# Kernel optimization log

Hardware: AMD Instinct MI355X
Metric: run time of the kernel (lower is better)

The kernel has to match this reference:

```python
import jax, jax.numpy as jnp
import numpy as np

EMBED_DIM = 1024
NUM_HEADS = 16
HEAD_DIM = EMBED_DIM // NUM_HEADS
B, T = 4, 1024
NEG = -1.0e9
LN_EPS = 1e-5


def setup_inputs() -> dict:
    key = jax.random.key(0)
    ks = jax.random.split(key, 13)
    s = 1.0 / np.sqrt(EMBED_DIM)
    return {
        "query": jax.random.normal(ks[0], (B, T, EMBED_DIM), jnp.float32),
        "key": jax.random.normal(ks[1], (B, T, EMBED_DIM), jnp.float32),
        "value": jax.random.normal(ks[2], (B, T, EMBED_DIM), jnp.float32),
        "mask": jax.random.randint(ks[3], (B, 1, T, T), 0, 2, jnp.int32),
        "Wq": jax.random.normal(ks[4], (EMBED_DIM, EMBED_DIM), jnp.float32) * s,
        "bq": jnp.zeros((EMBED_DIM,), jnp.float32),
        "Wk": jax.random.normal(ks[5], (EMBED_DIM, EMBED_DIM), jnp.float32) * s,
        "bk": jnp.zeros((EMBED_DIM,), jnp.float32),
        "Wv": jax.random.normal(ks[6], (EMBED_DIM, EMBED_DIM), jnp.float32) * s,
        "bv": jnp.zeros((EMBED_DIM,), jnp.float32),
        "Wo": jax.random.normal(ks[7], (EMBED_DIM, EMBED_DIM), jnp.float32) * s,
        "bo": jnp.zeros((EMBED_DIM,), jnp.float32),
        "gamma": jnp.ones((EMBED_DIM,), jnp.float32),
        "beta": jnp.zeros((EMBED_DIM,), jnp.float32),
    }


def _split_heads(x):
    # (B, T, E) -> (B, H, T, D)
    b, t, _ = x.shape
    return x.reshape(b, t, NUM_HEADS, HEAD_DIM).transpose(0, 2, 1, 3)


def _mha(query, key, value, mask, Wq, bq, Wk, bk, Wv, bv, Wo, bo, gamma, beta,
         temperature=1.0):
    q = _split_heads(query @ Wq.T + bq)
    k = _split_heads(key @ Wk.T + bk)
    v = _split_heads(value @ Wv.T + bv)
    # scores: (B, H, T, T)
    scale = jnp.sqrt(jnp.float32(HEAD_DIM)) * temperature
    scores = jnp.einsum("bhqd,bhkd->bhqk", q, k) / scale
    scores = jnp.where(mask == 0, NEG, scores)
    scores = scores - jnp.max(scores, axis=-1, keepdims=True)
    # temperature >= 0.01 in this config, so the low-temperature hard-cutoff
    # branch is skipped (matches torch's Python-level `if temperature < 0.01`).
    scores = jnp.nan_to_num(scores, nan=0.0, posinf=1.0e9, neginf=-1.0e9)
    attn = jax.nn.softmax(scores, axis=-1)
    # eval mode: dropout is identity (self.training is False)
    out = jnp.einsum("bhqk,bhkd->bhqd", attn, v)  # (B, H, T, D)
    out = out.transpose(0, 2, 1, 3).reshape(query.shape[0], query.shape[1], EMBED_DIM)
    out = out @ Wo.T + bo
    # layer norm over embed_dim
    mu = jnp.mean(out, axis=-1, keepdims=True)
    var = jnp.mean(jnp.square(out - mu), axis=-1, keepdims=True)
    out = (out - mu) * jax.lax.rsqrt(var + LN_EPS) * gamma + beta
    return out


def reference(query, key, value, mask, Wq, bq, Wk, bk, Wv, bv, Wo, bo, gamma, beta):
    return _mha(query, key, value, mask, Wq, bq, Wk, bk, Wv, bv, Wo, bo, gamma, beta)
```

## Files before the change

### kernel.cpp

```cpp
#include <hip/hip_runtime.h>
#include <cmath>

#define T_SEQ 1024
#define EMB   1024
#define NH    16
#define HD    64
#define NB    4
#define BQ    64
#define BK    64

#define QSCALE 0.18033688011112042f
#define BIAS2  -1.44269504e9f

using frag8   = __attribute__((ext_vector_type(8))) short;
using f32x4   = __attribute__((ext_vector_type(4))) float;
using short4v = __attribute__((ext_vector_type(4))) short;
using short8v = __attribute__((ext_vector_type(8))) short;

__device__ inline short f2bf(float f) {
    union { float f; unsigned u; } x; x.f = f;
    unsigned r = (x.u + 0x7FFFu + ((x.u >> 16) & 1u)) >> 16;
    return (short)r;
}
__device__ inline short f2bf_rhu(float f) {
    union { float f; unsigned u; } x; x.f = f;
    return (short)((x.u + 0x8000u) >> 16);
}
__device__ inline float bf2f(unsigned short u) {
    union { unsigned u; float f; } x; x.u = ((unsigned)u) << 16;
    return x.f;
}

__device__ inline void glds16(const short* g, short* l) {
    __builtin_amdgcn_global_load_lds(
        (const __attribute__((address_space(1))) void*)g,
        (__attribute__((address_space(3))) void*)l, 16, 0, 0);
}

struct ConvArgs { const float* src[7]; short* dst[7]; int n8[7]; };

__global__ __launch_bounds__(256) void convert_bf16(ConvArgs a) {
    const int y = blockIdx.y;
    const int t = blockIdx.x * 256 + threadIdx.x;
    if (t >= a.n8[y]) return;
    const float4* s = (const float4*)a.src[y];
    const float4 v0 = s[t * 2], v1 = s[t * 2 + 1];
    short8v o;
    o[0] = f2bf(v0.x); o[1] = f2bf(v0.y); o[2] = f2bf(v0.z); o[3] = f2bf(v0.w);
    o[4] = f2bf(v1.x); o[5] = f2bf(v1.y); o[6] = f2bf(v1.z); o[7] = f2bf(v1.w);
    *(short8v*)&a.dst[y][t * 8] = o;
}

__global__ __launch_bounds__(256) void convert_mask(
    const int* __restrict__ mask, short* __restrict__ dst)
{
    const int wave = threadIdx.x >> 6, lane = threadIdx.x & 63;
    const int tile = blockIdx.x * 4 + wave;
    const int bb   = tile >> 12;
    const int q16  = (tile >> 6) & 63;
    const int k16  = tile & 63;
    const int qrow = lane >> 2;
    const int col4 = (lane & 3) * 4;
    const int4 mv = *(const int4*)&mask[((size_t)bb * T_SEQ + q16 * 16 + qrow) * T_SEQ
                                        + k16 * 16 + col4];
    const short BB = f2bf(BIAS2);
    short4v o;
    o[0] = mv.x ? (short)0 : BB;
    o[1] = mv.y ? (short)0 : BB;
    o[2] = mv.z ? (short)0 : BB;
    o[3] = mv.w ? (short)0 : BB;
    *(short4v*)&dst[(size_t)tile * 256 + qrow * 16 + col4] = o;
}

struct GemmB { const short* A; const short* W; const float* bias; short* out; float scale; };
struct QkvArgs { GemmB g[3]; };

template <int MODE>
__device__ inline void gemm_core(const short* __restrict__ A,
                                 const short* __restrict__ W,
                                 const float* __restrict__ bias,
                                 float scale,
                                 short* __restrict__ outS,
                                 float* __restrict__ outF,
                                 int m0, int n0)
{
    __shared__ short As[2][128 * 32];
    __shared__ short Bs[2][128 * 32];

    const int tid  = threadIdx.x;
    const int wave = tid >> 6;
    const int lane = tid & 63;
    const int quad = lane >> 4;
    const int lm   = lane & 15;
    const int wr   = wave >> 1;
    const int wc   = wave & 1;
    const int K    = EMB;

    const int G0 = wave * 64 + lane, G1 = G0 + 256;
    const short* aSrc0 = A + (size_t)(m0 + (G0 >> 2)) * K + (G0 & 3) * 8;
    const short* aSrc1 = A + (size_t)(m0 + (G1 >> 2)) * K + (G1 & 3) * 8;
    const short* bSrc0 = W + (size_t)(n0 + (G0 >> 2)) * K + (G0 & 3) * 8;
    const short* bSrc1 = W + (size_t)(n0 + (G1 >> 2)) * K + (G1 & 3) * 8;
    short* aDst0 = &As[0][wave * 512];
    short* aDst1 = &As[0][2048 + wave * 512];
    short* bDst0 = &Bs[0][wave * 512];
    short* bDst1 = &Bs[0][2048 + wave * 512];

    f32x4 acc[4][4];
#pragma unroll
    for (int i = 0; i < 4; ++i)
#pragma unroll
        for (int j = 0; j < 4; ++j) acc[i][j] = (f32x4){0.f, 0.f, 0.f, 0.f};

    for (int kk = 0; kk < K; kk += 64) {
        __syncthreads();
        glds16(aSrc0 + kk,      aDst0);
        glds16(aSrc1 + kk,      aDst1);
        glds16(bSrc0 + kk,      bDst0);
        glds16(bSrc1 + kk,      bDst1);
        glds16(aSrc0 + kk + 32, aDst0 + 4096);
        glds16(aSrc1 + kk + 32, aDst1 + 4096);
        glds16(bSrc0 + kk + 32, bDst0 + 4096);
        glds16(bSrc1 + kk + 32, bDst1 + 4096);
        __syncthreads();

#pragma unroll
        for (int p = 0; p < 2; ++p) {
            frag8 aF[4], bF[4];
#pragma unroll
            for (int i = 0; i < 4; ++i)
                aF[i] = *(const frag8*)&As[p][(wr * 64 + i * 16 + lm) * 32 + quad * 8];
#pragma unroll
            for (int j = 0; j < 4; ++j)
                bF[j] = *(const frag8*)&Bs[p][(wc * 64 + j * 16 + lm) * 32 + quad * 8];
#pragma unroll
            for (int i = 0; i < 4; ++i)
#pragma unroll
                for (int j = 0; j < 4; ++j)
                    acc[i][j] = __builtin_amdgcn_mfma_f32_16x16x32_bf16(
                        aF[i], bF[j], acc[i][j], 0, 0, 0);
        }
    }

#pragma unroll
    for (int i = 0; i < 4; ++i)
#pragma unroll
        for (int j = 0; j < 4; ++j) {
            const int n = n0 + wc * 64 + j * 16 + lm;
            const float bv = bias[n];
#pragma unroll
            for (int rr = 0; rr < 4; ++rr) {
                const int m = m0 + wr * 64 + i * 16 + quad * 4 + rr;
                const float val = (acc[i][j][rr] + bv) * scale;
                if (MODE == 0) {
                    outF[((size_t)(m >> 4) * 64 + (n >> 4)) * 256 +
                         rr * 64 + quad * 16 + lm] = val;
                } else {
                    const int bb = m >> 10, tt = m & 1023;
                    const int h = n >> 6,  d  = n & 63;
                    const size_t bh = (size_t)bb * NH + h;
                    if (MODE == 1) {
                        outS[((bh * 64 + (tt >> 4)) * 8 + (d >> 3)) * 128 +
                             (tt & 15) * 8 + (d & 7)] = f2bf(val);
                    } else {
                        outS[((((bh * 16 + (tt >> 6)) * 2 + ((tt >> 5) & 1)) * 4 +
                              (d >> 4)) * 4 + ((tt >> 3) & 3)) * 128 +
                             (d & 15) * 8 + (tt & 7)] = f2bf(val);
                    }
                }
            }
        }
}

__global__ __launch_bounds__(256, 3) void gemm_qkv(QkvArgs args) {
    const int id = blockIdx.x + 8 * blockIdx.y + 256 * blockIdx.z;
    const int a  = id & 7;
    const int k2 = id >> 3;
    const int nb = k2 & 7;
    const int c  = k2 >> 3;
    const int pair = a * 12 + c;
    const int mb = pair & 31;
    const int zb = pair >> 5;
    const GemmB g = args.g[zb];
    if (zb < 2) gemm_core<1>(g.A, g.W, g.bias, g.scale, g.out, nullptr, mb * 128, nb * 128);
    else        gemm_core<2>(g.A, g.W, g.bias, g.scale, g.out, nullptr, mb * 128, nb * 128);
}

__global__ __launch_bounds__(256, 3) void gemm_wo(const short* __restrict__ A,
                                                  const short* __restrict__ W,
                                                  const float* __restrict__ bias,
                                                  float* __restrict__ out) {
    const int id = blockIdx.x + 8 * blockIdx.y;
    const int a  = id & 7;
    const int k2 = id >> 3;
    const int nb = k2 & 7;
    const int c  = k2 >> 3;
    const int mb = a * 4 + c;
    gemm_core<0>(A, W, bias, 1.0f, nullptr, out, mb * 128, nb * 128);
}

__global__ __launch_bounds__(256, 4) void flash_attn_mfma(
    const short* __restrict__ qf_, const short* __restrict__ kf_,
    const short* __restrict__ vf_, const short* __restrict__ mf_,
    short* __restrict__ out)
{
    __shared__ short Pl[4][2][16][72];

    const int tid  = threadIdx.x;
    const int wave = tid >> 6;
    const int lane = tid & 63;
    const int quad = lane >> 4;
    const int lm   = lane & 15;

    const int id  = blockIdx.x;
    const int xcd = id & 7;
    const int idx = id >> 3;
    const int bh_i = xcd * 8 + (idx >> 4);
    const int b  = bh_i >> 4, h = bh_i & 15;
    const int q0 = (idx & 15) * BQ;
    const size_t bh = (size_t)bh_i;

    const short* qb_ = qf_ + (bh * 64 + (q0 >> 4) + wave) * 1024;
    const frag8 qfa = *(const frag8*)&qb_[(quad * 16 + lm) * 8];
    const frag8 qfb = *(const frag8*)&qb_[((quad + 4) * 16 + lm) * 8];

    const short* mrow = mf_ + ((size_t)b * 64 + (q0 >> 4) + wave) * (64 * 256)
                        + lm * 16 + quad * 4;

    f32x4 of[4];
#pragma unroll
    for (int dc = 0; dc < 4; ++dc) of[dc] = (f32x4){0.f, 0.f, 0.f, 0.f};
    float lsum = 0.f;

    for (int kt2 = 0; kt2 < T_SEQ / BK; ++kt2) {
        const int pp = kt2 & 1;

        frag8 vf[2][4];
        const short* vbase = vf_ + (bh * 16 + kt2) * 4096;
#pragma unroll
        for (int kh2 = 0; kh2 < 2; ++kh2)
#pragma unroll
            for (int dc = 0; dc < 4; ++dc)
                vf[kh2][dc] = *(const frag8*)
                    &vbase[((kh2 * 4 + dc) * 4 + quad) * 128 + lm * 8];

        short4v mb[4];
#pragma unroll
        for (int kc = 0; kc < 4; ++kc)
            mb[kc] = *(const short4v*)&mrow[(kt2 * 4 + kc) * 256];

        f32x4 s[4];
#pragma unroll
        for (int kc = 0; kc < 4; ++kc) {
            const short* kbase = kf_ + (bh * 64 + kt2 * 4 + kc) * 1024;
            const frag8 kfa = *(const frag8*)&kbase[(quad * 16 + lm) * 8];
            const frag8 kfb = *(const frag8*)&kbase[((quad + 4) * 16 + lm) * 8];
            f32x4 a = (f32x4){ bf2f((unsigned short)mb[kc][0]),
                               bf2f((unsigned short)mb[kc][1]),
                               bf2f((unsigned short)mb[kc][2]),
                               bf2f((unsigned short)mb[kc][3]) };
            a = __builtin_amdgcn_mfma_f32_16x16x32_bf16(kfa, qfa, a, 0, 0, 0);
            a = __builtin_amdgcn_mfma_f32_16x16x32_bf16(kfb, qfb, a, 0, 0, 0);
            s[kc] = a;
        }

#pragma unroll
        for (int kc = 0; kc < 4; ++kc) {
            float p0 = exp2f(s[kc][0]), p1 = exp2f(s[kc][1]);
            float p2 = exp2f(s[kc][2]), p3 = exp2f(s[kc][3]);
            lsum += (p0 + p1) + (p2 + p3);
            short4v pk;
            pk[0] = f2bf_rhu(p0); pk[1] = f2bf_rhu(p1);
            pk[2] = f2bf_rhu(p2); pk[3] = f2bf_rhu(p3);
            *(short4v*)&Pl[wave][pp][lm][kc * 16 + quad * 4] = pk;
        }

        const frag8 pfa = *(const frag8*)&Pl[wave][pp][lm][quad * 8];
        const frag8 pfb = *(const frag8*)&Pl[wave][pp][lm][32 + quad * 8];
#pragma unroll
        for (int dc = 0; dc < 4; ++dc) {
            of[dc] = __builtin_amdgcn_mfma_f32_16x16x32_bf16(vf[0][dc], pfa, of[dc], 0, 0, 0);
            of[dc] = __builtin_amdgcn_mfma_f32_16x16x32_bf16(vf[1][dc], pfb, of[dc], 0, 0, 0);
        }
    }

    lsum += __shfl_xor(lsum, 16);
    lsum += __shfl_xor(lsum, 32);
    const float inv = 1.0f / lsum;

    short* ob = out + ((size_t)b * T_SEQ + q0 + wave * 16 + lm) * EMB + h * HD;
#pragma unroll
    for (int dc = 0; dc < 4; ++dc) {
        short4v o4;
#pragma unroll
        for (int rr = 0; rr < 4; ++rr) o4[rr] = f2bf(of[dc][rr] * inv);
        *(short4v*)&ob[dc * 16 + quad * 4] = o4;
    }
}

__global__ __launch_bounds__(256) void layernorm_k(
    const float* __restrict__ x, const float* __restrict__ gamma,
    const float* __restrict__ beta, float* __restrict__ out)
{
    __shared__ float ws1[4], ws2[4];
    const int tid = threadIdx.x;
    const int row = blockIdx.x;
    const int m16 = row >> 4, rr = row & 3, qd = (row >> 2) & 3;

    const float4 v = *(const float4*)&x[((size_t)m16 * 64 + (tid >> 2)) * 256 +
                                        rr * 64 + qd * 16 + (tid & 3) * 4];
    float s  = v.x + v.y + v.z + v.w;
    float ss = v.x * v.x + v.y * v.y + v.z * v.z + v.w * v.w;
#pragma unroll
    for (int off = 32; off > 0; off >>= 1) {
        s  += __shfl_down(s, off);
        ss += __shfl_down(ss, off);
    }
    if ((tid & 63) == 0) { ws1[tid >> 6] = s; ws2[tid >> 6] = ss; }
    __syncthreads();
    if (tid == 0) {
        const float a = ws1[0] + ws1[1] + ws1[2] + ws1[3];
        const float bsum = ws2[0] + ws2[1] + ws2[2] + ws2[3];
        const float mu = a * (1.0f / EMB);
        const float var = bsum * (1.0f / EMB) - mu * mu;
        ws1[0] = mu;
        ws2[0] = rsqrtf(var + 1e-5f);
    }
    __syncthreads();
    const float mu = ws1[0], rstd = ws2[0];

    const float4 g = *(const float4*)&gamma[tid * 4];
    const float4 bt = *(const float4*)&beta[tid * 4];
    float4 r;
    r.x = (v.x - mu) * rstd * g.x + bt.x;
    r.y = (v.y - mu) * rstd * g.y + bt.y;
    r.z = (v.z - mu) * rstd * g.z + bt.z;
    r.w = (v.w - mu) * rstd * g.w + bt.w;
    *(float4*)&out[(size_t)row * EMB + tid * 4] = r;
}

extern "C" void kernel_launch(void* const* d_in, const int* in_sizes, int n_in,
                              void* d_out, int out_size, void* d_ws, size_t ws_size,
                              hipStream_t stream) {
    const float* query = (const float*)d_in[0];
    const float* key_i = (const float*)d_in[1];
    const float* value = (const float*)d_in[2];
    const int*   mask  = (const int*)d_in[3];
    const float* Wq = (const float*)d_in[4];
    const float* bq = (const float*)d_in[5];
    const float* Wk = (const float*)d_in[6];
    const float* bk = (const float*)d_in[7];
    const float* Wv = (const float*)d_in[8];
    const float* bv = (const float*)d_in[9];
    const float* Wo = (const float*)d_in[10];
    const float* bo = (const float*)d_in[11];
    const float* gamma = (const float*)d_in[12];
    const float* beta  = (const float*)d_in[13];

    const size_t SZ = (size_t)NB * T_SEQ * EMB;
    const size_t WZ = (size_t)EMB * EMB;
    short* sws = (short*)d_ws;
    short* q_bf  = sws;
    short* k_bf  = sws + SZ;
    short* v_bf  = sws + 2 * SZ;
    short* w_bf  = sws + 3 * SZ;
    short* qh    = sws + 4 * SZ;
    short* kh    = sws + 5 * SZ;
    short* vh    = sws + 6 * SZ;
    short* maskb = sws + 7 * SZ;
    short* attnb = q_bf;
    float* projb = (float*)(sws + SZ);

    ConvArgs ca;
    ca.src[0] = query; ca.dst[0] = q_bf;          ca.n8[0] = (int)(SZ / 8);
    ca.src[1] = key_i; ca.dst[1] = k_bf;          ca.n8[1] = (int)(SZ / 8);
    ca.src[2] = value; ca.dst[2] = v_bf;          ca.n8[2] = (int)(SZ / 8);
    ca.src[3] = Wq;    ca.dst[3] = w_bf;          ca.n8[3] = (int)(WZ / 8);
    ca.src[4] = Wk;    ca.dst[4] = w_bf + WZ;     ca.n8[4] = (int)(WZ / 8);
    ca.src[5] = Wv;    ca.dst[5] = w_bf + 2 * WZ; ca.n8[5] = (int)(WZ / 8);
    ca.src[6] = Wo;    ca.dst[6] = w_bf + 3 * WZ; ca.n8[6] = (int)(WZ / 8);
    convert_bf16<<<dim3((SZ / 8 + 255) / 256, 7), 256, 0, stream>>>(ca);

    convert_mask<<<dim3(NB * 64 * 64 / 4), 256, 0, stream>>>(mask, maskb);

    QkvArgs qa;
    qa.g[0] = { q_bf, w_bf,          bq, qh, QSCALE };
    qa.g[1] = { k_bf, w_bf + WZ,     bk, kh, 1.0f };
    qa.g[2] = { v_bf, w_bf + 2 * WZ, bv, vh, 1.0f };
    gemm_qkv<<<dim3(EMB / 128, NB * T_SEQ / 128, 3), 256, 0, stream>>>(qa);

    flash_attn_mfma<<<dim3(T_SEQ / BQ * NH * NB), 256, 0, stream>>>(qh, kh, vh, maskb, attnb);

    gemm_wo<<<dim3(EMB / 128, NB * T_SEQ / 128), 256, 0, stream>>>(
        attnb, w_bf + 3 * WZ, bo, projb);

    layernorm_k<<<dim3(NB * T_SEQ), 256, 0, stream>>>(projb, gamma, beta, (float*)d_out);
}
```

Before: 258.7 us.

## Software-pipeline GEMM global loads via registers and prefetch K/mask tiles in attention

The GEMM core drops direct global-to-LDS loads in favour of register-staged double buffering. The next K-slice is loaded into registers while MFMAs run on the current LDS buffer, then stored to the other buffer, with one barrier per 32-wide step. The flash attention kernel now prefetches the next K tile and mask fragments one iteration ahead, and its occupancy hint is lowered from 4 to 3 blocks to make room for the extra registers. The aim is to hide global memory latency behind compute, at the cost of higher register pressure and possibly lower occupancy.

New measurement: 273.3 us. 5.6% more time.

```diff
diff --git a/kernel.cpp b/kernel.cpp
--- a/kernel.cpp
+++ b/kernel.cpp
@@ -29,12 +29,6 @@
 __device__ inline float bf2f(unsigned short u) {
     union { unsigned u; float f; } x; x.u = ((unsigned)u) << 16;
     return x.f;
-}
-
-__device__ inline void glds16(const short* g, short* l) {
-    __builtin_amdgcn_global_load_lds(
-        (const __attribute__((address_space(1))) void*)g,
-        (__attribute__((address_space(3))) void*)l, 16, 0, 0);
 }
 
 struct ConvArgs { const float* src[7]; short* dst[7]; int n8[7]; };
@@ -75,6 +69,44 @@
 struct GemmB { const short* A; const short* W; const float* bias; short* out; float scale; };
 struct QkvArgs { GemmB g[3]; };
 
+__device__ __forceinline__ void k_step(
+    const short (&AsP)[128 * 32], const short (&BsP)[128 * 32],
+    short (&AsN)[128 * 32], short (&BsN)[128 * 32],
+    const short* aSrc0, const short* aSrc1,
+    const short* bSrc0, const short* bSrc1,
+    int loadOff, bool doLoad, bool doStore,
+    short8v (&rLoad)[4], short8v (&rStore)[4],
+    int G0, int G1, int wr, int wc, int lm, int quad,
+    f32x4 (&acc)[4][4])
+{
+    if (doLoad) {
+        rLoad[0] = *(const short8v*)(aSrc0 + loadOff);
+        rLoad[1] = *(const short8v*)(aSrc1 + loadOff);
+        rLoad[2] = *(const short8v*)(bSrc0 + loadOff);
+        rLoad[3] = *(const short8v*)(bSrc1 + loadOff);
+    }
+    frag8 aF[4], bF[4];
+#pragma unroll
+    for (int i = 0; i < 4; ++i)
+        aF[i] = *(const frag8*)&AsP[(wr * 64 + i * 16 + lm) * 32 + quad * 8];
+#pragma unroll
+    for (int j = 0; j < 4; ++j)
+        bF[j] = *(const frag8*)&BsP[(wc * 64 + j * 16 + lm) * 32 + quad * 8];
+#pragma unroll
+    for (int i = 0; i < 4; ++i)
+#pragma unroll
+        for (int j = 0; j < 4; ++j)
+            acc[i][j] = __builtin_amdgcn_mfma_f32_16x16x32_bf16(
+                aF[i], bF[j], acc[i][j], 0, 0, 0);
+    if (doStore) {
+        *(short8v*)&AsN[G0 * 8] = rStore[0];
+        *(short8v*)&AsN[G1 * 8] = rStore[1];
+        *(short8v*)&BsN[G0 * 8] = rStore[2];
+        *(short8v*)&BsN[G1 * 8] = rStore[3];
+        __syncthreads();
+    }
+}
+
 template <int MODE>
 __device__ inline void gemm_core(const short* __restrict__ A,
                                  const short* __restrict__ W,
@@ -101,10 +133,6 @@
     const short* aSrc1 = A + (size_t)(m0 + (G1 >> 2)) * K + (G1 & 3) * 8;
     const short* bSrc0 = W + (size_t)(n0 + (G0 >> 2)) * K + (G0 & 3) * 8;
     const short* bSrc1 = W + (size_t)(n0 + (G1 >> 2)) * K + (G1 & 3) * 8;
-    short* aDst0 = &As[0][wave * 512];
-    short* aDst1 = &As[0][2048 + wave * 512];
-    short* bDst0 = &Bs[0][wave * 512];
-    short* bDst1 = &Bs[0][2048 + wave * 512];
 
     f32x4 acc[4][4];
 #pragma unroll
@@ -112,34 +140,29 @@
 #pragma unroll
         for (int j = 0; j < 4; ++j) acc[i][j] = (f32x4){0.f, 0.f, 0.f, 0.f};
 
-    for (int kk = 0; kk < K; kk += 64) {
-        __syncthreads();
-        glds16(aSrc0 + kk,      aDst0);
-        glds16(aSrc1 + kk,      aDst1);
-        glds16(bSrc0 + kk,      bDst0);
-        glds16(bSrc1 + kk,      bDst1);
-        glds16(aSrc0 + kk + 32, aDst0 + 4096);
-        glds16(aSrc1 + kk + 32, aDst1 + 4096);
-        glds16(bSrc0 + kk + 32, bDst0 + 4096);
-        glds16(bSrc1 + kk + 32, bDst1 + 4096);
-        __syncthreads();
-
-#pragma unroll
-        for (int p = 0; p < 2; ++p) {
-            frag8 aF[4], bF[4];
-#pragma unroll
-            for (int i = 0; i < 4; ++i)
-                aF[i] = *(const frag8*)&As[p][(wr * 64 + i * 16 + lm) * 32 + quad * 8];
-#pragma unroll
-            for (int j = 0; j < 4; ++j)
-                bF[j] = *(const frag8*)&Bs[p][(wc * 64 + j * 16 + lm) * 32 + quad * 8];
-#pragma unroll
-            for (int i = 0; i < 4; ++i)
-#pragma unroll
-                for (int j = 0; j < 4; ++j)
-                    acc[i][j] = __builtin_amdgcn_mfma_f32_16x16x32_bf16(
-                        aF[i], bF[j], acc[i][j], 0, 0, 0);
-        }
+    short8v r0[4], r1[4];
+    r0[0] = *(const short8v*)(aSrc0);
+    r0[1] = *(const short8v*)(aSrc1);
+    r0[2] = *(const short8v*)(bSrc0);
+    r0[3] = *(const short8v*)(bSrc1);
+    *(short8v*)&As[0][G0 * 8] = r0[0];
+    *(short8v*)&As[0][G1 * 8] = r0[1];
+    *(short8v*)&Bs[0][G0 * 8] = r0[2];
+    *(short8v*)&Bs[0][G1 * 8] = r0[3];
+    r1[0] = *(const short8v*)(aSrc0 + 32);
+    r1[1] = *(const short8v*)(aSrc1 + 32);
+    r1[2] = *(const short8v*)(bSrc0 + 32);
+    r1[3] = *(const short8v*)(bSrc1 + 32);
+    __syncthreads();
+
+    const int NP = K / 32;
+    for (int i = 0; i < NP; i += 2) {
+        k_step(As[0], Bs[0], As[1], Bs[1], aSrc0, aSrc1, bSrc0, bSrc1,
+               (i + 2) * 32, i + 2 < NP, true, r0, r1,
+               G0, G1, wr, wc, lm, quad, acc);
+        k_step(As[1], Bs[1], As[0], Bs[0], aSrc0, aSrc1, bSrc0, bSrc1,
+               (i + 3) * 32, i + 3 < NP, i + 2 < NP, r1, r0,
+               G0, G1, wr, wc, lm, quad, acc);
     }
 
 #pragma unroll
@@ -199,7 +222,7 @@
     gemm_core<0>(A, W, bias, 1.0f, nullptr, out, mb * 128, nb * 128);
 }
 
-__global__ __launch_bounds__(256, 4) void flash_attn_mfma(
+__global__ __launch_bounds__(256, 3) void flash_attn_mfma(
     const short* __restrict__ qf_, const short* __restrict__ kf_,
     const short* __restrict__ vf_, const short* __restrict__ mf_,
     short* __restrict__ out)
@@ -232,11 +255,20 @@
     for (int dc = 0; dc < 4; ++dc) of[dc] = (f32x4){0.f, 0.f, 0.f, 0.f};
     float lsum = 0.f;
 
-    for (int kt2 = 0; kt2 < T_SEQ / BK; ++kt2) {
-        const int pp = kt2 & 1;
-
+    auto load_kt = [&](int kt, frag8 (&kA)[4], frag8 (&kB)[4], short4v (&mm)[4]) {
+#pragma unroll
+        for (int kc = 0; kc < 4; ++kc) {
+            const short* kbase = kf_ + (bh * 64 + kt * 4 + kc) * 1024;
+            kA[kc] = *(const frag8*)&kbase[(quad * 16 + lm) * 8];
+            kB[kc] = *(const frag8*)&kbase[((quad + 4) * 16 + lm) * 8];
+            mm[kc] = *(const short4v*)&mrow[(kt * 4 + kc) * 256];
+        }
+    };
+
+    auto tile = [&](int kt, int pp, frag8 (&kA)[4], frag8 (&kB)[4],
+                    short4v (&mm)[4]) {
         frag8 vf[2][4];
-        const short* vbase = vf_ + (bh * 16 + kt2) * 4096;
+        const short* vbase = vf_ + (bh * 16 + kt) * 4096;
 #pragma unroll
         for (int kh2 = 0; kh2 < 2; ++kh2)
 #pragma unroll
@@ -244,23 +276,15 @@
                 vf[kh2][dc] = *(const frag8*)
                     &vbase[((kh2 * 4 + dc) * 4 + quad) * 128 + lm * 8];
 
-        short4v mb[4];
-#pragma unroll
-        for (int kc = 0; kc < 4; ++kc)
-            mb[kc] = *(const short4v*)&mrow[(kt2 * 4 + kc) * 256];
-
         f32x4 s[4];
 #pragma unroll
         for (int kc = 0; kc < 4; ++kc) {
-            const short* kbase = kf_ + (bh * 64 + kt2 * 4 + kc) * 1024;
-            const frag8 kfa = *(const frag8*)&kbase[(quad * 16 + lm) * 8];
-            const frag8 kfb = *(const frag8*)&kbase[((quad + 4) * 16 + lm) * 8];
-            f32x4 a = (f32x4){ bf2f((unsigned short)mb[kc][0]),
-                               bf2f((unsigned short)mb[kc][1]),
-                               bf2f((unsigned short)mb[kc][2]),
-                               bf2f((unsigned short)mb[kc][3]) };
-            a = __builtin_amdgcn_mfma_f32_16x16x32_bf16(kfa, qfa, a, 0, 0, 0);
-            a = __builtin_amdgcn_mfma_f32_16x16x32_bf16(kfb, qfb, a, 0, 0, 0);
+            f32x4 a = (f32x4){ bf2f((unsigned short)mm[kc][0]),
+                               bf2f((unsigned short)mm[kc][1]),
+                               bf2f((unsigned short)mm[kc][2]),
+                               bf2f((unsigned short)mm[kc][3]) };
+            a = __builtin_amdgcn_mfma_f32_16x16x32_bf16(kA[kc], qfa, a, 0, 0, 0);
+            a = __builtin_amdgcn_mfma_f32_16x16x32_bf16(kB[kc], qfb, a, 0, 0, 0);
             s[kc] = a;
         }
 
@@ -282,6 +306,17 @@
             of[dc] = __builtin_amdgcn_mfma_f32_16x16x32_bf16(vf[0][dc], pfa, of[dc], 0, 0, 0);
             of[dc] = __builtin_amdgcn_mfma_f32_16x16x32_bf16(vf[1][dc], pfb, of[dc], 0, 0, 0);
         }
+    };
+
+    frag8 kA0[4], kB0[4], kA1[4], kB1[4];
+    short4v m0[4], m1[4];
+    load_kt(0, kA0, kB0, m0);
+    for (int kt = 0; kt < T_SEQ / BK; kt += 2) {
+        load_kt(kt + 1, kA1, kB1, m1);
+        tile(kt, 0, kA0, kB0, m0);
+        if (kt + 2 < T_SEQ / BK)
+            load_kt(kt + 2, kA0, kB0, m0);
+        tile(kt + 1, 1, kA1, kB1, m1);
     }
 
     lsum += __shfl_xor(lsum, 16);
```
